# Kernel optimization log

Measured on AMD Instinct MI355X. Metric: run time of the kernel, lower is better.

Reference implementation:

```python
import jax, jax.numpy as jnp
import numpy as np

RANK = 16
NUM_STEPS = 10
STEP_SIZE = 1000.0
INIT_SCALE = 1e-3


def _init(k, shape):
    # projection of Dirichlet-like init onto sphere neighborhood: center +- init_scale uniform noise
    center = 1.0 / np.sqrt(shape[-1])
    return (center + (2.0 * INIT_SCALE) * jax.random.uniform(k, shape, dtype=jnp.float32) - INIT_SCALE)


def setup_inputs() -> dict:
    key = jax.random.key(0)
    ks = jax.random.split(key, 5)
    B, H, S, D = 2, 12, 8192, 64
    query = jax.random.normal(ks[0], (B, H, S, D), dtype=jnp.float32)
    key_t = jax.random.normal(ks[1], (B, H, S, D), dtype=jnp.float32)
    value = jax.random.normal(ks[2], (B, H, S, D), dtype=jnp.float32)
    left_params = _init(ks[3], (B, H, S, RANK))
    right_params = _init(ks[4], (B, H, RANK, S))
    return {"query": query, "key": key_t, "value": value,
            "left_params": left_params, "right_params": right_params}


def _unit(x):
    return x / jnp.linalg.norm(x, axis=-1, keepdims=True)


def _grad(lp, rp, q, k, inv_s2):
    # lp: [..., S, r]  rp: [..., r, S]  q,k: [..., S, D]
    ls = _unit(lp)
    rs = _unit(rp)
    L = ls * ls   # left simplex factor  [..., S, r]
    R = rs * rs   # right simplex factor [..., r, S]

    # d_left = (L (R R^T) - Q (K^T R^T)) / S^2   -- contract small dims first, never SxS
    RR = jnp.einsum('...ki,...li->...kl', R, R)          # [r, r]
    KR = jnp.einsum('...ia,...li->...la', k, R)          # [r, D]
    dl = (jnp.einsum('...jk,...kl->...jl', L, RR)
          - jnp.einsum('...ja,...la->...jl', q, KR)) * inv_s2
    dl = dl * 2.0 * ls
    dl = dl - ls * jnp.sum(ls * dl, axis=-1, keepdims=True)   # tangent-space projection
    dl = dl / jnp.linalg.norm(lp, axis=-1, keepdims=True)

    # d_right = ((L^T L) R - (L^T Q) K^T) / S^2
    LL = jnp.einsum('...jk,...jl->...kl', L, L)          # [r, r]
    LQ = jnp.einsum('...jk,...ja->...ka', L, q)          # [r, D]
    dr = (jnp.einsum('...kl,...li->...ki', LL, R)
          - jnp.einsum('...ka,...ia->...ki', LQ, k)) * inv_s2
    dr = dr * 2.0 * rs
    dr = dr - rs * jnp.sum(rs * dr, axis=-1, keepdims=True)
    dr = dr / jnp.linalg.norm(rp, axis=-1, keepdims=True)
    return dl, dr


def _forward(query, key, value, left_params, right_params):
    S = query.shape[-2]
    inv_s2 = jnp.float32(1.0 / (S * S))

    def step(carry, _):
        lp, rp = carry
        dl, dr = _grad(lp, rp, query, key, inv_s2)
        return (lp - STEP_SIZE * dl, rp - STEP_SIZE * dr), None

    (lp, rp), _ = jax.lax.scan(step, (left_params, right_params), None, length=NUM_STEPS)
    left = _unit(lp) ** 2    # [..., S, r]
    right = _unit(rp) ** 2   # [..., r, S]
    # left @ (right @ value) -- rank-bottleneck multiply, O(S*r*D)
    rv = jnp.einsum('...ki,...id->...kd', right, value)
    return jnp.einsum('...jk,...kd->...jd', left, rv)


def reference(query, key, value, left_params, right_params):
    return _forward(query, key, value, left_params, right_params)
```

## Files before the change

### kernel.cpp

```cpp
#include <hip/hip_runtime.h>

#define S_ 8192
#define D_ 64
#define BH_ 24

static constexpr float INV_S2 = 1.0f / (8192.0f * 8192.0f);
static constexpr float STEPSZ = 1000.0f;
static constexpr float CC = 2.0f * INV_S2;

#define LP_N (BH_ * S_ * 16)
#define PART_STRIDE 2576
#define PART_N (BH_ * 32 * PART_STRIDE)
#define ACCF_STRIDE 2624
#define ACCF_N (BH_ * ACCF_STRIDE)
#define PART2_STRIDE 1040
#define PART2_N (BH_ * 32 * PART2_STRIDE)

#define STG 20
#define WK_OFF 2608
#define LDS_FLOATS (WK_OFF + 5600)

template <int KIND>
__device__ __forceinline__ void reduceSideW(const float* __restrict__ sb, int j0, int t,
                                            const float* vals, float* WK,
                                            float* __restrict__ pbase) {
  const int lane = t & 63, w = t >> 6, tcx = t & 15;
  {
    float4* st = (float4*)(WK + t * STG);
    st[0] = make_float4(vals[0], vals[1], vals[2], vals[3]);
    st[1] = make_float4(vals[4], vals[5], vals[6], vals[7]);
    st[2] = make_float4(vals[8], vals[9], vals[10], vals[11]);
    st[3] = make_float4(vals[12], vals[13], vals[14], vals[15]);
  }
  __syncthreads();
  float aQ[16], aX[16], aN[16];
#pragma unroll
  for (int l = 0; l < 16; ++l) { aQ[l] = 0.f; aX[l] = 0.f; aN[l] = 0.f; }
#pragma unroll 4
  for (int it = 0; it < 64; ++it) {
    const int jl = (w << 6) + it;
    const float4* Vw = (const float4*)(WK + jl * STG);
    float4 b0 = Vw[0], b1 = Vw[1], b2 = Vw[2], b3 = Vw[3];
    float Vv[16] = {b0.x,b0.y,b0.z,b0.w, b1.x,b1.y,b1.z,b1.w,
                    b2.x,b2.y,b2.z,b2.w, b3.x,b3.y,b3.z,b3.w};
    float xq = sb[(size_t)(j0 + jl) * D_ + lane];
    float xc = (KIND < 2) ? WK[jl * STG + tcx] : 0.f;
#pragma unroll
    for (int l = 0; l < 16; ++l) {
      aQ[l] += Vv[l] * xq;
      if (KIND < 2) aX[l] += Vv[l] * xc;
      if (KIND >= 1) aN[l] += Vv[l];
    }
  }
  __syncthreads();
  float* rg = WK + w * 1400;
  {
    float* p = rg + lane * 17;
#pragma unroll
    for (int l = 0; l < 16; ++l) p[l] = aQ[l];
  }
  if (KIND < 2 && lane < 16) {
    float* p = rg + 1088 + lane * 17;
#pragma unroll
    for (int l = 0; l < 16; ++l) p[l] = aX[l];
  }
  if (KIND >= 1 && lane == 0) {
#pragma unroll
    for (int l = 0; l < 16; ++l) rg[1360 + l] = aN[l];
  }
  __syncthreads();
#pragma unroll
  for (int r = 0; r < 4; ++r) {
    int o = t + r * 256;
    int a = o >> 4, l = o & 15;
    int idx = a * 17 + l;
    pbase[a * 16 + l] = WK[idx] + WK[1400 + idx] + WK[2800 + idx] + WK[4200 + idx];
  }
  if (KIND < 2) {
    int c = t >> 4, l = t & 15;
    int idx = 1088 + c * 17 + l;
    pbase[1024 + l * 16 + c] = WK[idx] + WK[1400 + idx] + WK[2800 + idx] + WK[4200 + idx];
  }
  if (KIND >= 1 && t < 16) {
    int idx = 1360 + t;
    pbase[(KIND == 1 ? 1280 : 1024) + t] =
        WK[idx] + WK[1400 + idx] + WK[2800 + idx] + WK[4200 + idx];
  }
  __syncthreads();
}

__device__ __forceinline__ void rowUpdate(const float* M, const float4* q4, float lv[16]) {
  const float4* RR4 = (const float4*)M;
  const float4* KR4 = (const float4*)(M + 256);
  float n2 = 0.f;
#pragma unroll
  for (int l = 0; l < 16; ++l) n2 += lv[l] * lv[l];
  float ri = rsqrtf(n2);
  float ls[16], L[16];
#pragma unroll
  for (int l = 0; l < 16; ++l) { ls[l] = lv[l] * ri; L[l] = ls[l] * ls[l]; }
  float dl[16];
#pragma unroll
  for (int l = 0; l < 16; ++l) dl[l] = 0.f;
#pragma unroll
  for (int k = 0; k < 16; ++k) {
    float Lk = L[k];
#pragma unroll
    for (int g = 0; g < 4; ++g) {
      float4 rr = RR4[k * 4 + g];
      dl[4*g+0] += Lk * rr.x; dl[4*g+1] += Lk * rr.y;
      dl[4*g+2] += Lk * rr.z; dl[4*g+3] += Lk * rr.w;
    }
  }
#pragma unroll
  for (int a4 = 0; a4 < 16; ++a4) {
    float4 qq = q4[a4];
#pragma unroll
    for (int c = 0; c < 4; ++c) {
      float qa = (c == 0) ? qq.x : (c == 1) ? qq.y : (c == 2) ? qq.z : qq.w;
      int a = a4 * 4 + c;
#pragma unroll
      for (int g = 0; g < 4; ++g) {
        float4 kr = KR4[a * 4 + g];
        dl[4*g+0] -= qa * kr.x; dl[4*g+1] -= qa * kr.y;
        dl[4*g+2] -= qa * kr.z; dl[4*g+3] -= qa * kr.w;
      }
    }
  }
  float dot = 0.f;
#pragma unroll
  for (int l = 0; l < 16; ++l) { dl[l] *= ls[l]; dot += ls[l] * dl[l]; }
#pragma unroll
  for (int l = 0; l < 16; ++l) lv[l] -= STEPSZ * (dl[l] - ls[l] * dot) * ri;
}

__device__ __forceinline__ void colUpdateB(const float* M, const float* C,
                                           const float4* k4, float nv[16]) {
  const float4* MLL4 = (const float4*)M;
  const float4* MLQ4 = (const float4*)(M + 256);
  const float* C1 = C;
  const float* C2 = C + 16;
  const float* SRN = C + 32;
  float rp2[16];
#pragma unroll
  for (int l = 0; l < 16; ++l) rp2[l] = nv[l] * nv[l];
  float s[16];
#pragma unroll
  for (int k = 0; k < 16; ++k) {
    float a0 = 0.f;
#pragma unroll
    for (int g = 0; g < 4; ++g) {
      float4 m = MLL4[k * 4 + g];
      a0 += m.x * rp2[4*g+0] + m.y * rp2[4*g+1] + m.z * rp2[4*g+2] + m.w * rp2[4*g+3];
    }
    s[k] = a0;
  }
#pragma unroll
  for (int a4 = 0; a4 < 16; ++a4) {
    float4 kk = k4[a4];
#pragma unroll
    for (int k = 0; k < 16; ++k) {
      float4 m = MLQ4[k * 16 + a4];
      s[k] -= m.x * kk.x + m.y * kk.y + m.z * kk.z + m.w * kk.w;
    }
  }
#pragma unroll
  for (int k = 0; k < 16; ++k) {
    float rs = nv[k] * SRN[k];
    float d2 = rs * s[k];
    nv[k] = C1[k] * nv[k] - C2[k] * d2;
  }
}

template <int MODE>
__global__ void __launch_bounds__(256) kStep(const float* __restrict__ accF,
                                             const float* __restrict__ q,
                                             const float* __restrict__ key,
                                             const float* __restrict__ vv,
                                             const float* __restrict__ lp0,
                                             const float* __restrict__ rp0,
                                             float* __restrict__ lp,
                                             float* __restrict__ rp,
                                             float* __restrict__ part,
                                             float* __restrict__ part2) {
  const int bh = blockIdx.y, bx = blockIdx.x, t = threadIdx.x;
  const int j0 = bx * 256, j = j0 + t;
  const int bb = bh * 32 + bx;
  __shared__ float B[LDS_FLOATS];
  float* MAT = B;
  float* WK = B + WK_OFF;
  const float* A = accF + (size_t)bh * ACCF_STRIDE;
  const float* qb = q + (size_t)bh * S_ * D_;
  const float* kb = key + (size_t)bh * S_ * D_;
  const size_t base = ((size_t)bh * S_ + j) * 16;

  if (MODE >= 1) {
    for (int e = t; e < 2608; e += 256) MAT[e] = A[e];
    __syncthreads();
  }

  {
    float lv[16];
    const float4* s4 = (const float4*)((MODE == 0 ? lp0 : lp) + base);
    float4 a0 = s4[0], a1 = s4[1], a2 = s4[2], a3 = s4[3];
    lv[0]=a0.x; lv[1]=a0.y; lv[2]=a0.z; lv[3]=a0.w;
    lv[4]=a1.x; lv[5]=a1.y; lv[6]=a1.z; lv[7]=a1.w;
    lv[8]=a2.x; lv[9]=a2.y; lv[10]=a2.z; lv[11]=a2.w;
    lv[12]=a3.x; lv[13]=a3.y; lv[14]=a3.z; lv[15]=a3.w;
    if (MODE >= 1) {
      rowUpdate(MAT + 1280, (const float4*)(qb + (size_t)j * D_), lv);
    }
    float4* d4 = (float4*)(lp + base);
    d4[0] = make_float4(lv[0], lv[1], lv[2], lv[3]);
    d4[1] = make_float4(lv[4], lv[5], lv[6], lv[7]);
    d4[2] = make_float4(lv[8], lv[9], lv[10], lv[11]);
    d4[3] = make_float4(lv[12], lv[13], lv[14], lv[15]);
    if (MODE < 2) {
      float L[16];
      float m2 = 0.f;
#pragma unroll
      for (int l = 0; l < 16; ++l) m2 += lv[l] * lv[l];
      float r2 = 1.0f / m2;
#pragma unroll
      for (int l = 0; l < 16; ++l) L[l] = lv[l] * lv[l] * r2;
      reduceSideW<0>(qb, j0, t, L, WK, part + (size_t)bb * PART_STRIDE);
    }
  }

  {
    float nv[16];
    if (MODE == 0) {
      const float* rsrc = rp0 + (size_t)bh * 16 * S_ + j;
#pragma unroll
      for (int k = 0; k < 16; ++k) nv[k] = rsrc[(size_t)k * S_];
    } else {
      const float4* r4 = (const float4*)(rp + base);
      float4 a0 = r4[0], a1 = r4[1], a2 = r4[2], a3 = r4[3];
      nv[0]=a0.x; nv[1]=a0.y; nv[2]=a0.z; nv[3]=a0.w;
      nv[4]=a1.x; nv[5]=a1.y; nv[6]=a1.z; nv[7]=a1.w;
      nv[8]=a2.x; nv[9]=a2.y; nv[10]=a2.z; nv[11]=a2.w;
      nv[12]=a3.x; nv[13]=a3.y; nv[14]=a3.z; nv[15]=a3.w;
      colUpdateB(MAT, MAT + 2560, (const float4*)(kb + (size_t)j * D_), nv);
    }
    float4* d4 = (float4*)(rp + base);
    d4[0] = make_float4(nv[0], nv[1], nv[2], nv[3]);
    d4[1] = make_float4(nv[4], nv[5], nv[6], nv[7]);
    d4[2] = make_float4(nv[8], nv[9], nv[10], nv[11]);
    d4[3] = make_float4(nv[12], nv[13], nv[14], nv[15]);
    float rp2[16];
#pragma unroll
    for (int l = 0; l < 16; ++l) rp2[l] = nv[l] * nv[l];
    if (MODE < 2)
      reduceSideW<1>(kb, j0, t, rp2, WK, part + (size_t)bb * PART_STRIDE + 1280);
    else
      reduceSideW<2>(vv + (size_t)bh * S_ * D_, j0, t, rp2, WK,
                     part2 + (size_t)bb * PART2_STRIDE);
  }
}

__global__ void __launch_bounds__(256) kB(const float* __restrict__ part,
                                          float* __restrict__ accF) {
  const int bh = blockIdx.x, t = threadIdx.x;
  __shared__ float raw[PART_STRIDE];
  __shared__ float inn[16], srn[16];
  const float* p0 = part + (size_t)bh * 32 * PART_STRIDE;
  for (int vI = t; vI < PART_STRIDE; vI += 256) {
    float s = 0.f;
    const float* p = p0 + vI;
#pragma unroll 8
    for (int b2 = 0; b2 < 32; ++b2) s += p[(size_t)b2 * PART_STRIDE];
    raw[vI] = s;
  }
  __syncthreads();
  if (t < 16) {
    float N = raw[2560 + t];
    inn[t] = 1.0f / N;
    srn[t] = rsqrtf(N);
  }
  __syncthreads();
  float* o = accF + (size_t)bh * ACCF_STRIDE;
  o[t] = raw[1024 + t] * CC * inn[t & 15];
  o[1280 + t] = raw[2304 + t] * CC * inn[t >> 4] * inn[t & 15];
#pragma unroll
  for (int r = 0; r < 4; ++r) {
    int e = t + r * 256;
    o[256 + e] = raw[((e & 63) << 4) + (e >> 6)] * CC;
  }
#pragma unroll
  for (int r = 0; r < 4; ++r) {
    int e = t + r * 256;
    o[1536 + e] = raw[1280 + e] * CC * inn[e & 15];
  }
  if (t < 16) {
    int k = t;
    float s = 0.f;
#pragma unroll
    for (int l = 0; l < 16; ++l)
      s += raw[1024 + k * 16 + l] * CC * inn[l] * raw[2304 + k * 16 + l];
#pragma unroll
    for (int a = 0; a < 64; ++a)
      s -= raw[a * 16 + k] * CC * raw[1280 + a * 16 + k];
    float PJ = inn[k] * s;
    o[2560 + t] = 1.0f + STEPSZ * PJ * inn[t];
    o[2576 + t] = STEPSZ * srn[t];
    o[2592 + t] = srn[t];
  }
}

__global__ void __launch_bounds__(256) kBF(const float* __restrict__ part2,
                                           float* __restrict__ RVs) {
  const int bh = blockIdx.x, t = threadIdx.x;
  __shared__ float raw[PART2_STRIDE];
  __shared__ float inn[16];
  const float* p0 = part2 + (size_t)bh * 32 * PART2_STRIDE;
  for (int vI = t; vI < PART2_STRIDE; vI += 256) {
    float s = 0.f;
    const float* p = p0 + vI;
#pragma unroll 8
    for (int b2 = 0; b2 < 32; ++b2) s += p[(size_t)b2 * PART2_STRIDE];
    raw[vI] = s;
  }
  __syncthreads();
  if (t < 16) inn[t] = 1.0f / raw[1024 + t];
  __syncthreads();
#pragma unroll
  for (int r = 0; r < 4; ++r) {
    int e = t + r * 256;
    RVs[(size_t)bh * 1024 + e] = raw[((e & 63) << 4) + (e >> 6)] * inn[e >> 6];
  }
}

__global__ void __launch_bounds__(256) kOut(const float* __restrict__ lp,
                                            const float* __restrict__ RVs,
                                            float* __restrict__ out) {
  const int bh = blockIdx.y, t = threadIdx.x;
  __shared__ float rvs[1024];
#pragma unroll
  for (int r = 0; r < 4; ++r) rvs[t + r * 256] = RVs[(size_t)bh * 1024 + t + r * 256];
  __syncthreads();
  const int j = blockIdx.x * 256 + t;
  size_t base = ((size_t)bh * S_ + j) * 16;
  const float4* lp4 = (const float4*)(lp + base);
  float4 a0 = lp4[0], a1 = lp4[1], a2 = lp4[2], a3 = lp4[3];
  float lv[16] = {a0.x,a0.y,a0.z,a0.w, a1.x,a1.y,a1.z,a1.w,
                  a2.x,a2.y,a2.z,a2.w, a3.x,a3.y,a3.z,a3.w};
  float n2 = 0.f;
#pragma unroll
  for (int l = 0; l < 16; ++l) n2 += lv[l] * lv[l];
  float r2 = 1.0f / n2;
  float L[16];
#pragma unroll
  for (int l = 0; l < 16; ++l) L[l] = lv[l] * lv[l] * r2;
  float o[64];
#pragma unroll
  for (int d = 0; d < 64; ++d) o[d] = 0.f;
  const float4* rv4 = (const float4*)rvs;
#pragma unroll
  for (int k = 0; k < 16; ++k) {
    float Lk = L[k];
#pragma unroll
    for (int d4 = 0; d4 < 16; ++d4) {
      float4 r = rv4[k * 16 + d4];
      o[4*d4+0] += Lk * r.x; o[4*d4+1] += Lk * r.y;
      o[4*d4+2] += Lk * r.z; o[4*d4+3] += Lk * r.w;
    }
  }
  float4* o4 = (float4*)(out + ((size_t)bh * S_ + j) * D_);
#pragma unroll
  for (int d4 = 0; d4 < 16; ++d4)
    o4[d4] = make_float4(o[4*d4+0], o[4*d4+1], o[4*d4+2], o[4*d4+3]);
}

extern "C" void kernel_launch(void* const* d_in, const int* in_sizes, int n_in,
                              void* d_out, int out_size, void* d_ws, size_t ws_size,
                              hipStream_t stream) {
  (void)in_sizes; (void)n_in; (void)out_size; (void)ws_size;
  const float* q = (const float*)d_in[0];
  const float* key = (const float*)d_in[1];
  const float* v = (const float*)d_in[2];
  const float* lp0 = (const float*)d_in[3];
  const float* rp0 = (const float*)d_in[4];
  float* out = (float*)d_out;
  float* ws = (float*)d_ws;

  float* lp = ws;
  float* rp = lp + LP_N;
  float* part = rp + LP_N;
  float* accF = part + PART_N;
  float* part2 = accF + ACCF_N;
  float* RVs = part2 + PART2_N;

  dim3 blk(256);
  dim3 gS(32, BH_);
  kStep<0><<<gS, blk, 0, stream>>>(accF, q, key, v, lp0, rp0, lp, rp, part, part2);
  for (int s = 0; s < 10; ++s) {
    kB<<<dim3(BH_), blk, 0, stream>>>(part, accF);
    if (s < 9)
      kStep<1><<<gS, blk, 0, stream>>>(accF, q, key, v, lp0, rp0, lp, rp, part, part2);
    else
      kStep<2><<<gS, blk, 0, stream>>>(accF, q, key, v, lp0, rp0, lp, rp, part, part2);
  }
  kBF<<<dim3(BH_), blk, 0, stream>>>(part2, RVs);
  kOut<<<gS, blk, 0, stream>>>(lp, RVs, out);
}
```

Measured before the change: 935.1 us.

## Transpose Q/K and factors to column-major, split row/col work across grid z

Adds pre-pass kernels that transpose query, key and the left params so per-thread reads in the update loops are coalesced across threads instead of strided 256-byte rows. The row and column updates now run in separate blocks (grid z=2), which doubles parallelism and cuts LDS per block. The reduction is also restructured so the 16-wide X/N sums use a strided row split plus wavefront shuffles instead of full 64-row loops. The cost is extra transpose traffic, more workspace (the transposed path is used only when the workspace is large enough), and a layout change to the KR/LQ matrices read in kB.

```diff
diff --git a/kernel.cpp b/kernel.cpp
--- a/kernel.cpp
+++ b/kernel.cpp
@@ -9,6 +9,7 @@
 static constexpr float CC = 2.0f * INV_S2;
 
 #define LP_N (BH_ * S_ * 16)
+#define QT_N (BH_ * S_ * 64)
 #define PART_STRIDE 2576
 #define PART_N (BH_ * 32 * PART_STRIDE)
 #define ACCF_STRIDE 2624
@@ -17,43 +18,59 @@
 #define PART2_N (BH_ * 32 * PART2_STRIDE)
 
 #define STG 20
-#define WK_OFF 2608
-#define LDS_FLOATS (WK_OFF + 5600)
 
 template <int KIND>
 __device__ __forceinline__ void reduceSideW(const float* __restrict__ sb, int j0, int t,
-                                            const float* vals, float* WK,
+                                            const float* vals, float* B,
                                             float* __restrict__ pbase) {
-  const int lane = t & 63, w = t >> 6, tcx = t & 15;
+  const int lane = t & 63, w = t >> 6, tcx = t & 15, rr = (t >> 4) & 3;
   {
-    float4* st = (float4*)(WK + t * STG);
+    float4* st = (float4*)(B + t * STG);
     st[0] = make_float4(vals[0], vals[1], vals[2], vals[3]);
     st[1] = make_float4(vals[4], vals[5], vals[6], vals[7]);
     st[2] = make_float4(vals[8], vals[9], vals[10], vals[11]);
     st[3] = make_float4(vals[12], vals[13], vals[14], vals[15]);
   }
   __syncthreads();
-  float aQ[16], aX[16], aN[16];
-#pragma unroll
-  for (int l = 0; l < 16; ++l) { aQ[l] = 0.f; aX[l] = 0.f; aN[l] = 0.f; }
-#pragma unroll 4
+  float aQ[16];
+#pragma unroll
+  for (int l = 0; l < 16; ++l) aQ[l] = 0.f;
+  const float* srow = sb + (size_t)(j0 + (w << 6)) * D_ + lane;
+#pragma unroll 8
   for (int it = 0; it < 64; ++it) {
     const int jl = (w << 6) + it;
-    const float4* Vw = (const float4*)(WK + jl * STG);
+    const float4* Vw = (const float4*)(B + jl * STG);
+    float4 b0 = Vw[0], b1 = Vw[1], b2 = Vw[2], b3 = Vw[3];
+    float xq = srow[(size_t)it * D_];
+    aQ[0]  += b0.x * xq; aQ[1]  += b0.y * xq; aQ[2]  += b0.z * xq; aQ[3]  += b0.w * xq;
+    aQ[4]  += b1.x * xq; aQ[5]  += b1.y * xq; aQ[6]  += b1.z * xq; aQ[7]  += b1.w * xq;
+    aQ[8]  += b2.x * xq; aQ[9]  += b2.y * xq; aQ[10] += b2.z * xq; aQ[11] += b2.w * xq;
+    aQ[12] += b3.x * xq; aQ[13] += b3.y * xq; aQ[14] += b3.z * xq; aQ[15] += b3.w * xq;
+  }
+  float aX[16], aN[16];
+#pragma unroll
+  for (int l = 0; l < 16; ++l) { aX[l] = 0.f; aN[l] = 0.f; }
+#pragma unroll 4
+  for (int it = 0; it < 16; ++it) {
+    const int jl = (w << 6) + rr + (it << 2);
+    const float4* Vw = (const float4*)(B + jl * STG);
     float4 b0 = Vw[0], b1 = Vw[1], b2 = Vw[2], b3 = Vw[3];
     float Vv[16] = {b0.x,b0.y,b0.z,b0.w, b1.x,b1.y,b1.z,b1.w,
                     b2.x,b2.y,b2.z,b2.w, b3.x,b3.y,b3.z,b3.w};
-    float xq = sb[(size_t)(j0 + jl) * D_ + lane];
-    float xc = (KIND < 2) ? WK[jl * STG + tcx] : 0.f;
+    float xc = (KIND < 2) ? B[jl * STG + tcx] : 0.f;
 #pragma unroll
     for (int l = 0; l < 16; ++l) {
-      aQ[l] += Vv[l] * xq;
       if (KIND < 2) aX[l] += Vv[l] * xc;
       if (KIND >= 1) aN[l] += Vv[l];
     }
   }
-  __syncthreads();
-  float* rg = WK + w * 1400;
+#pragma unroll
+  for (int l = 0; l < 16; ++l) {
+    if (KIND < 2) { float v = aX[l]; v += __shfl_xor(v, 16); v += __shfl_xor(v, 32); aX[l] = v; }
+    if (KIND >= 1) { float v = aN[l]; v += __shfl_xor(v, 16); v += __shfl_xor(v, 32); aN[l] = v; }
+  }
+  __syncthreads();
+  float* rg = B + w * 1400;
   {
     float* p = rg + lane * 17;
 #pragma unroll
@@ -74,24 +91,25 @@
     int o = t + r * 256;
     int a = o >> 4, l = o & 15;
     int idx = a * 17 + l;
-    pbase[a * 16 + l] = WK[idx] + WK[1400 + idx] + WK[2800 + idx] + WK[4200 + idx];
+    pbase[a * 16 + l] = B[idx] + B[1400 + idx] + B[2800 + idx] + B[4200 + idx];
   }
   if (KIND < 2) {
     int c = t >> 4, l = t & 15;
     int idx = 1088 + c * 17 + l;
-    pbase[1024 + l * 16 + c] = WK[idx] + WK[1400 + idx] + WK[2800 + idx] + WK[4200 + idx];
+    pbase[1024 + l * 16 + c] = B[idx] + B[1400 + idx] + B[2800 + idx] + B[4200 + idx];
   }
   if (KIND >= 1 && t < 16) {
     int idx = 1360 + t;
     pbase[(KIND == 1 ? 1280 : 1024) + t] =
-        WK[idx] + WK[1400 + idx] + WK[2800 + idx] + WK[4200 + idx];
-  }
-  __syncthreads();
-}
-
-__device__ __forceinline__ void rowUpdate(const float* M, const float4* q4, float lv[16]) {
+        B[idx] + B[1400 + idx] + B[2800 + idx] + B[4200 + idx];
+  }
+  __syncthreads();
+}
+
+template <int UT>
+__device__ __forceinline__ void rowUpdate(const float* M, const float* __restrict__ qsrc,
+                                          int j, float lv[16]) {
   const float4* RR4 = (const float4*)M;
-  const float4* KR4 = (const float4*)(M + 256);
   float n2 = 0.f;
 #pragma unroll
   for (int l = 0; l < 16; ++l) n2 += lv[l] * lv[l];
@@ -112,20 +130,35 @@
       dl[4*g+2] += Lk * rr.z; dl[4*g+3] += Lk * rr.w;
     }
   }
-#pragma unroll
-  for (int a4 = 0; a4 < 16; ++a4) {
-    float4 qq = q4[a4];
-#pragma unroll
-    for (int c = 0; c < 4; ++c) {
-      float qa = (c == 0) ? qq.x : (c == 1) ? qq.y : (c == 2) ? qq.z : qq.w;
-      int a = a4 * 4 + c;
+  if (UT) {
+#pragma unroll 8
+    for (int a = 0; a < 64; ++a) {
+      float qa = qsrc[(size_t)a * S_ + j];
+      const float4* kr = (const float4*)(M + 256 + a * 16);
 #pragma unroll
       for (int g = 0; g < 4; ++g) {
-        float4 kr = KR4[a * 4 + g];
-        dl[4*g+0] -= qa * kr.x; dl[4*g+1] -= qa * kr.y;
-        dl[4*g+2] -= qa * kr.z; dl[4*g+3] -= qa * kr.w;
+        float4 k4 = kr[g];
+        dl[4*g+0] -= qa * k4.x; dl[4*g+1] -= qa * k4.y;
+        dl[4*g+2] -= qa * k4.z; dl[4*g+3] -= qa * k4.w;
       }
     }
+  } else {
+    const float4* q4 = (const float4*)qsrc;
+#pragma unroll
+    for (int a4 = 0; a4 < 16; ++a4) {
+      float4 qq = q4[a4];
+#pragma unroll
+      for (int c = 0; c < 4; ++c) {
+        float qa = (c == 0) ? qq.x : (c == 1) ? qq.y : (c == 2) ? qq.z : qq.w;
+        const float4* kr = (const float4*)(M + 256 + (a4 * 4 + c) * 16);
+#pragma unroll
+        for (int g = 0; g < 4; ++g) {
+          float4 k4 = kr[g];
+          dl[4*g+0] -= qa * k4.x; dl[4*g+1] -= qa * k4.y;
+          dl[4*g+2] -= qa * k4.z; dl[4*g+3] -= qa * k4.w;
+        }
+      }
+    }
   }
   float dot = 0.f;
 #pragma unroll
@@ -134,10 +167,11 @@
   for (int l = 0; l < 16; ++l) lv[l] -= STEPSZ * (dl[l] - ls[l] * dot) * ri;
 }
 
-__device__ __forceinline__ void colUpdateB(const float* M, const float* C,
-                                           const float4* k4, float nv[16]) {
+template <int UT>
+__device__ __forceinline__ void colUpdate(const float* M, const float* C,
+                                          const float* __restrict__ ksrc,
+                                          int i, float nv[16]) {
   const float4* MLL4 = (const float4*)M;
-  const float4* MLQ4 = (const float4*)(M + 256);
   const float* C1 = C;
   const float* C2 = C + 16;
   const float* SRN = C + 32;
@@ -155,13 +189,34 @@
     }
     s[k] = a0;
   }
-#pragma unroll
-  for (int a4 = 0; a4 < 16; ++a4) {
-    float4 kk = k4[a4];
-#pragma unroll
-    for (int k = 0; k < 16; ++k) {
-      float4 m = MLQ4[k * 16 + a4];
-      s[k] -= m.x * kk.x + m.y * kk.y + m.z * kk.z + m.w * kk.w;
+  if (UT) {
+#pragma unroll 8
+    for (int a = 0; a < 64; ++a) {
+      float ka = ksrc[(size_t)a * S_ + i];
+      const float4* mq = (const float4*)(M + 256 + a * 16);
+#pragma unroll
+      for (int g = 0; g < 4; ++g) {
+        float4 m = mq[g];
+        s[4*g+0] -= ka * m.x; s[4*g+1] -= ka * m.y;
+        s[4*g+2] -= ka * m.z; s[4*g+3] -= ka * m.w;
+      }
+    }
+  } else {
+    const float4* k4 = (const float4*)ksrc;
+#pragma unroll
+    for (int a4 = 0; a4 < 16; ++a4) {
+      float4 kk = k4[a4];
+#pragma unroll
+      for (int c = 0; c < 4; ++c) {
+        float ka = (c == 0) ? kk.x : (c == 1) ? kk.y : (c == 2) ? kk.z : kk.w;
+        const float4* mq = (const float4*)(M + 256 + (a4 * 4 + c) * 16);
+#pragma unroll
+        for (int g = 0; g < 4; ++g) {
+          float4 m = mq[g];
+          s[4*g+0] -= ka * m.x; s[4*g+1] -= ka * m.y;
+          s[4*g+2] -= ka * m.z; s[4*g+3] -= ka * m.w;
+        }
+      }
     }
   }
 #pragma unroll
@@ -172,88 +227,71 @@
   }
 }
 
-template <int MODE>
+template <int MODE, int UT>
 __global__ void __launch_bounds__(256) kStep(const float* __restrict__ accF,
                                              const float* __restrict__ q,
                                              const float* __restrict__ key,
                                              const float* __restrict__ vv,
-                                             const float* __restrict__ lp0,
-                                             const float* __restrict__ rp0,
-                                             float* __restrict__ lp,
-                                             float* __restrict__ rp,
+                                             const float* __restrict__ qT,
+                                             const float* __restrict__ kT,
+                                             float* __restrict__ lpT,
+                                             const float* __restrict__ rp_src,
+                                             float* __restrict__ rp_dst,
                                              float* __restrict__ part,
                                              float* __restrict__ part2) {
   const int bh = blockIdx.y, bx = blockIdx.x, t = threadIdx.x;
   const int j0 = bx * 256, j = j0 + t;
   const int bb = bh * 32 + bx;
-  __shared__ float B[LDS_FLOATS];
-  float* MAT = B;
-  float* WK = B + WK_OFF;
+  __shared__ float B[6400];
   const float* A = accF + (size_t)bh * ACCF_STRIDE;
   const float* qb = q + (size_t)bh * S_ * D_;
   const float* kb = key + (size_t)bh * S_ * D_;
-  const size_t base = ((size_t)bh * S_ + j) * 16;
-
-  if (MODE >= 1) {
-    for (int e = t; e < 2608; e += 256) MAT[e] = A[e];
-    __syncthreads();
-  }
-
-  {
+
+  if (blockIdx.z == 0) {
+    float* lpb = lpT + (size_t)bh * 16 * S_;
     float lv[16];
-    const float4* s4 = (const float4*)((MODE == 0 ? lp0 : lp) + base);
-    float4 a0 = s4[0], a1 = s4[1], a2 = s4[2], a3 = s4[3];
-    lv[0]=a0.x; lv[1]=a0.y; lv[2]=a0.z; lv[3]=a0.w;
-    lv[4]=a1.x; lv[5]=a1.y; lv[6]=a1.z; lv[7]=a1.w;
-    lv[8]=a2.x; lv[9]=a2.y; lv[10]=a2.z; lv[11]=a2.w;
-    lv[12]=a3.x; lv[13]=a3.y; lv[14]=a3.z; lv[15]=a3.w;
+#pragma unroll
+    for (int l = 0; l < 16; ++l) lv[l] = lpb[(size_t)l * S_ + j];
     if (MODE >= 1) {
-      rowUpdate(MAT + 1280, (const float4*)(qb + (size_t)j * D_), lv);
-    }
-    float4* d4 = (float4*)(lp + base);
-    d4[0] = make_float4(lv[0], lv[1], lv[2], lv[3]);
-    d4[1] = make_float4(lv[4], lv[5], lv[6], lv[7]);
-    d4[2] = make_float4(lv[8], lv[9], lv[10], lv[11]);
-    d4[3] = make_float4(lv[12], lv[13], lv[14], lv[15]);
-    if (MODE < 2) {
-      float L[16];
+      for (int e = t; e < 1280; e += 256) B[e] = A[1280 + e];
+      __syncthreads();
+      rowUpdate<UT>(B, UT ? (qT + (size_t)bh * 64 * S_) : (qb + (size_t)j * D_), j, lv);
+#pragma unroll
+      for (int l = 0; l < 16; ++l) lpb[(size_t)l * S_ + j] = lv[l];
+      if (MODE == 2) return;
+      __syncthreads();
+    }
+    float L[16];
+    {
       float m2 = 0.f;
 #pragma unroll
       for (int l = 0; l < 16; ++l) m2 += lv[l] * lv[l];
       float r2 = 1.0f / m2;
 #pragma unroll
       for (int l = 0; l < 16; ++l) L[l] = lv[l] * lv[l] * r2;
-      reduceSideW<0>(qb, j0, t, L, WK, part + (size_t)bb * PART_STRIDE);
-    }
-  }
-
-  {
+    }
+    reduceSideW<0>(qb, j0, t, L, B, part + (size_t)bb * PART_STRIDE);
+  } else {
+    const float* rsb = rp_src + (size_t)bh * 16 * S_;
     float nv[16];
-    if (MODE == 0) {
-      const float* rsrc = rp0 + (size_t)bh * 16 * S_ + j;
-#pragma unroll
-      for (int k = 0; k < 16; ++k) nv[k] = rsrc[(size_t)k * S_];
-    } else {
-      const float4* r4 = (const float4*)(rp + base);
-      float4 a0 = r4[0], a1 = r4[1], a2 = r4[2], a3 = r4[3];
-      nv[0]=a0.x; nv[1]=a0.y; nv[2]=a0.z; nv[3]=a0.w;
-      nv[4]=a1.x; nv[5]=a1.y; nv[6]=a1.z; nv[7]=a1.w;
-      nv[8]=a2.x; nv[9]=a2.y; nv[10]=a2.z; nv[11]=a2.w;
-      nv[12]=a3.x; nv[13]=a3.y; nv[14]=a3.z; nv[15]=a3.w;
-      colUpdateB(MAT, MAT + 2560, (const float4*)(kb + (size_t)j * D_), nv);
-    }
-    float4* d4 = (float4*)(rp + base);
-    d4[0] = make_float4(nv[0], nv[1], nv[2], nv[3]);
-    d4[1] = make_float4(nv[4], nv[5], nv[6], nv[7]);
-    d4[2] = make_float4(nv[8], nv[9], nv[10], nv[11]);
-    d4[3] = make_float4(nv[12], nv[13], nv[14], nv[15]);
+#pragma unroll
+    for (int k = 0; k < 16; ++k) nv[k] = rsb[(size_t)k * S_ + j];
+    if (MODE >= 1) {
+      for (int e = t; e < 1328; e += 256) B[e] = (e < 1280) ? A[e] : A[1280 + e];
+      __syncthreads();
+      colUpdate<UT>(B, B + 1280, UT ? (kT + (size_t)bh * 64 * S_) : (kb + (size_t)j * D_), j, nv);
+      float* rdb = rp_dst + (size_t)bh * 16 * S_;
+#pragma unroll
+      for (int k = 0; k < 16; ++k) rdb[(size_t)k * S_ + j] = nv[k];
+      __syncthreads();
+    }
     float rp2[16];
 #pragma unroll
     for (int l = 0; l < 16; ++l) rp2[l] = nv[l] * nv[l];
     if (MODE < 2)
-      reduceSideW<1>(kb, j0, t, rp2, WK, part + (size_t)bb * PART_STRIDE + 1280);
+      reduceSideW<1>(kb, j0, t, rp2, B, part + (size_t)bb * PART_STRIDE + 1280);
     else
-      reduceSideW<2>(vv + (size_t)bh * S_ * D_, j0, t, rp2, WK,
+      reduceSideW<2>(vv + (size_t)bh * S_ * D_, j0, t, rp2, B,
                      part2 + (size_t)bb * PART2_STRIDE);
   }
 }
@@ -284,7 +322,7 @@
 #pragma unroll
   for (int r = 0; r < 4; ++r) {
     int e = t + r * 256;
-    o[256 + e] = raw[((e & 63) << 4) + (e >> 6)] * CC;
+    o[256 + e] = raw[e] * CC;
   }
 #pragma unroll
   for (int r = 0; r < 4; ++r) {
@@ -330,7 +368,7 @@
   }
 }
 
-__global__ void __launch_bounds__(256) kOut(const float* __restrict__ lp,
+__global__ void __launch_bounds__(256) kOut(const float* __restrict__ lpT,
                                             const float* __restrict__ RVs,
                                             float* __restrict__ out) {
   const int bh = blockIdx.y, t = threadIdx.x;
@@ -339,11 +377,10 @@
   for (int r = 0; r < 4; ++r) rvs[t + r * 256] = RVs[(size_t)bh * 1024 + t + r * 256];
   __syncthreads();
   const int j = blockIdx.x * 256 + t;
-  size_t base = ((size_t)bh * S_ + j) * 16;
-  const float4* lp4 = (const float4*)(lp + base);
-  float4 a0 = lp4[0], a1 = lp4[1], a2 = lp4[2], a3 = lp4[3];
-  float lv[16] = {a0.x,a0.y,a0.z,a0.w, a1.x,a1.y,a1.z,a1.w,
-                  a2.x,a2.y,a2.z,a2.w, a3.x,a3.y,a3.z,a3.w};
+  const float* lpb = lpT + (size_t)bh * 16 * S_;
+  float lv[16];
+#pragma unroll
+  for (int l = 0; l < 16; ++l) lv[l] = lpb[(size_t)l * S_ + j];
   float n2 = 0.f;
 #pragma unroll
   for (int l = 0; l < 16; ++l) n2 += lv[l] * lv[l];
@@ -371,10 +408,50 @@
     o4[d4] = make_float4(o[4*d4+0], o[4*d4+1], o[4*d4+2], o[4*d4+3]);
 }
 
+__global__ void __launch_bounds__(256) kTrans64(const float* __restrict__ src,
+                                                float* __restrict__ dst) {
+  const int bh = blockIdx.y, t = threadIdx.x;
+  const int j0 = blockIdx.x * 64;
+  __shared__ float tile[64 * 65];
+#pragma unroll
+  for (int i = 0; i < 16; ++i) {
+    int idx = t + 256 * i;
+    int row = idx >> 6, col = idx & 63;
+    tile[col * 65 + row] = src[((size_t)bh * S_ + j0 + row) * 64 + col];
+  }
+  __syncthreads();
+#pragma unroll
+  for (int i = 0; i < 16; ++i) {
+    int idx = t + 256 * i;
+    int a = idx >> 6, jj = idx & 63;
+    dst[(size_t)bh * 64 * S_ + (size_t)a * S_ + j0 + jj] = tile[a * 65 + jj];
+  }
+}
+
+__global__ void __launch_bounds__(256) kTransL(const float* __restrict__ lp0,
+                                               float* __restrict__ lpT) {
+  const int bh = blockIdx.y, t = threadIdx.x;
+  const int j0 = blockIdx.x * 64;
+  __shared__ float tile[16 * 65];
+#pragma unroll
+  for (int i = 0; i < 4; ++i) {
+    int idx = t + 256 * i;
+    int row = idx >> 4, col = idx & 15;
+    tile[col * 65 + row] = lp0[((size_t)bh * S_ + j0 + row) * 16 + col];
+  }
+  __syncthreads();
+#pragma unroll
+  for (int i = 0; i < 4; ++i) {
+    int idx = t + 256 * i;
+    int l = idx >> 6, jj = idx & 63;
+    lpT[(size_t)bh * 16 * S_ + (size_t)l * S_ + j0 + jj] = tile[l * 65 + jj];
+  }
+}
+
 extern "C" void kernel_launch(void* const* d_in, const int* in_sizes, int n_in,
                               void* d_out, int out_size, void* d_ws, size_t ws_size,
                               hipStream_t stream) {
-  (void)in_sizes; (void)n_in; (void)out_size; (void)ws_size;
+  (void)in_sizes; (void)n_in; (void)out_size;
   const float* q = (const float*)d_in[0];
   const float* key = (const float*)d_in[1];
   const float* v = (const float*)d_in[2];
@@ -383,23 +460,48 @@
   float* out = (float*)d_out;
   float* ws = (float*)d_ws;
 
-  float* lp = ws;
-  float* rp = lp + LP_N;
+  float* lpT = ws;
+  float* rp = lpT + LP_N;
   float* part = rp + LP_N;
   float* accF = part + PART_N;
   float* part2 = accF + ACCF_N;
   float* RVs = part2 + PART2_N;
+  float* qT = RVs + BH_ * 1024;
+  float* kT = qT + QT_N;
+  const size_t full_need = (size_t)(9156096 + 2 * QT_N) * sizeof(float);
+  const bool useT = ws_size >= full_need;
 
   dim3 blk(256);
-  dim3 gS(32, BH_);
-  kStep<0><<<gS, blk, 0, stream>>>(accF, q, key, v, lp0, rp0, lp, rp, part, part2);
-  for (int s = 0; s < 10; ++s) {
-    kB<<<dim3(BH_), blk, 0, stream>>>(part, accF);
-    if (s < 9)
-      kStep<1><<<gS, blk, 0, stream>>>(accF, q, key, v, lp0, rp0, lp, rp, part, part2);
-    else
-      kStep<2><<<gS, blk, 0, stream>>>(accF, q, key, v, lp0, rp0, lp, rp, part, part2);
+  dim3 gS(32, BH_, 2);
+  dim3 gT(128, BH_);
+
+  kTransL<<<gT, blk, 0, stream>>>(lp0, lpT);
+  if (useT) {
+    kTrans64<<<gT, blk, 0, stream>>>(q, qT);
+    kTrans64<<<gT, blk, 0, stream>>>(key, kT);
+  }
+
+  if (useT) {
+    kStep<0, 1><<<gS, blk, 0, stream>>>(accF, q, key, v, qT, kT, lpT, rp0, rp, part, part2);
+    for (int s = 0; s < 10; ++s) {
+      kB<<<dim3(BH_), blk, 0, stream>>>(part, accF);
+      const float* rsrc = (s == 0) ? rp0 : rp;
+      if (s < 9)
+        kStep<1, 1><<<gS, blk, 0, stream>>>(accF, q, key, v, qT, kT, lpT, rsrc, rp, part, part2);
+      else
+        kStep<2, 1><<<gS, blk, 0, stream>>>(accF, q, key, v, qT, kT, lpT, rsrc, rp, part, part2);
+    }
+  } else {
+    kStep<0, 0><<<gS, blk, 0, stream>>>(accF, q, key, v, qT, kT, lpT, rp0, rp, part, part2);
+    for (int s = 0; s < 10; ++s) {
+      kB<<<dim3(BH_), blk, 0, stream>>>(part, accF);
+      const float* rsrc = (s == 0) ? rp0 : rp;
+      if (s < 9)
+        kStep<1, 0><<<gS, blk, 0, stream>>>(accF, q, key, v, qT, kT, lpT, rsrc, rp, part, part2);
+      else
+        kStep<2, 0><<<gS, blk, 0, stream>>>(accF, q, key, v, qT, kT, lpT, rsrc, rp, part, part2);
+    }
   }
   kBF<<<dim3(BH_), blk, 0, stream>>>(part2, RVs);
-  kOut<<<gS, blk, 0, stream>>>(lp, RVs, out);
-}
+  kOut<<<dim3(32, BH_), blk, 0, stream>>>(lpT, RVs, out);
+}
```

Result: slower. 1.303 ms (+39.3%).

## Split row and column updates into separate blocks and restructure reductions

Applied to the files above, without the earlier changes.

The step kernel's grid gains a z dimension: z=0 blocks handle left-factor rows and z=1 blocks handle right-factor columns, and each block now covers 512 positions in two halves. The Q/K-weighted side reduction is reorganized so each thread accumulates a 4x16 outer product from float4 loads and partial sums are combined with cross-lane shuffles instead of extra LDS passes. The KR/LQ matrix layout in accF is transposed so the row and column updates read contiguous float4 rows, and kB writes those entries untransposed. The intent is more parallel blocks per step, fewer barriers and fewer LDS round trips, at the cost of more registers per thread and each block loading its own copy of the small matrices.

```diff
diff --git a/kernel.cpp b/kernel.cpp
--- a/kernel.cpp
+++ b/kernel.cpp
@@ -16,48 +16,81 @@
 #define PART2_STRIDE 1040
 #define PART2_N (BH_ * 32 * PART2_STRIDE)
 
-#define STG 20
-#define WK_OFF 2608
-#define LDS_FLOATS (WK_OFF + 5600)
-
 template <int KIND>
-__device__ __forceinline__ void reduceSideW(const float* __restrict__ sb, int j0, int t,
-                                            const float* vals, float* WK,
-                                            float* __restrict__ pbase) {
-  const int lane = t & 63, w = t >> 6, tcx = t & 15;
+__device__ __forceinline__ void reduceSide(const float* __restrict__ sb, int jbase, int t,
+                                           const float* vals, float* ST, float* RD,
+                                           float* __restrict__ pbase) {
+  const int tc = t & 15, trw = t >> 4, w = t >> 6, lane = t & 63;
   {
-    float4* st = (float4*)(WK + t * STG);
+    float4* st = (float4*)(ST + t * 20);
     st[0] = make_float4(vals[0], vals[1], vals[2], vals[3]);
     st[1] = make_float4(vals[4], vals[5], vals[6], vals[7]);
     st[2] = make_float4(vals[8], vals[9], vals[10], vals[11]);
     st[3] = make_float4(vals[12], vals[13], vals[14], vals[15]);
   }
   __syncthreads();
-  float aQ[16], aX[16], aN[16];
-#pragma unroll
-  for (int l = 0; l < 16; ++l) { aQ[l] = 0.f; aX[l] = 0.f; aN[l] = 0.f; }
+  float aQ[4][16];
+#pragma unroll
+  for (int c = 0; c < 4; ++c)
+#pragma unroll
+    for (int l = 0; l < 16; ++l) aQ[c][l] = 0.f;
+  const float* srow = sb + (size_t)jbase * D_;
 #pragma unroll 4
-  for (int it = 0; it < 64; ++it) {
-    const int jl = (w << 6) + it;
-    const float4* Vw = (const float4*)(WK + jl * STG);
+  for (int it = 0; it < 16; ++it) {
+    const int jl = trw + (it << 4);
+    const float4* Vw = (const float4*)(ST + jl * 20);
     float4 b0 = Vw[0], b1 = Vw[1], b2 = Vw[2], b3 = Vw[3];
     float Vv[16] = {b0.x,b0.y,b0.z,b0.w, b1.x,b1.y,b1.z,b1.w,
                     b2.x,b2.y,b2.z,b2.w, b3.x,b3.y,b3.z,b3.w};
-    float xq = sb[(size_t)(j0 + jl) * D_ + lane];
-    float xc = (KIND < 2) ? WK[jl * STG + tcx] : 0.f;
+    float4 qq = *(const float4*)(srow + (size_t)jl * D_ + (tc << 2));
 #pragma unroll
     for (int l = 0; l < 16; ++l) {
-      aQ[l] += Vv[l] * xq;
+      aQ[0][l] += qq.x * Vv[l];
+      aQ[1][l] += qq.y * Vv[l];
+      aQ[2][l] += qq.z * Vv[l];
+      aQ[3][l] += qq.w * Vv[l];
+    }
+  }
+#pragma unroll
+  for (int c = 0; c < 4; ++c)
+#pragma unroll
+    for (int l = 0; l < 16; ++l) {
+      float v = aQ[c][l];
+      v += __shfl_xor(v, 16);
+      v += __shfl_xor(v, 32);
+      aQ[c][l] = v;
+    }
+  float* rg = RD + w * 1400;
+  if (lane < 16) {
+#pragma unroll
+    for (int c = 0; c < 4; ++c) {
+      float* p = rg + (4 * lane + c) * 17;
+#pragma unroll
+      for (int l = 0; l < 16; ++l) p[l] = aQ[c][l];
+    }
+  }
+  const int rr = trw & 3;
+  float aX[16], aN[16];
+#pragma unroll
+  for (int l = 0; l < 16; ++l) { aX[l] = 0.f; aN[l] = 0.f; }
+#pragma unroll 4
+  for (int it = 0; it < 16; ++it) {
+    const int jl = (w << 6) + rr + (it << 2);
+    const float4* Vw = (const float4*)(ST + jl * 20);
+    float4 b0 = Vw[0], b1 = Vw[1], b2 = Vw[2], b3 = Vw[3];
+    float Vv[16] = {b0.x,b0.y,b0.z,b0.w, b1.x,b1.y,b1.z,b1.w,
+                    b2.x,b2.y,b2.z,b2.w, b3.x,b3.y,b3.z,b3.w};
+    float xc = (KIND < 2) ? ST[jl * 20 + tc] : 0.f;
+#pragma unroll
+    for (int l = 0; l < 16; ++l) {
       if (KIND < 2) aX[l] += Vv[l] * xc;
       if (KIND >= 1) aN[l] += Vv[l];
     }
   }
-  __syncthreads();
-  float* rg = WK + w * 1400;
-  {
-    float* p = rg + lane * 17;
-#pragma unroll
-    for (int l = 0; l < 16; ++l) p[l] = aQ[l];
+#pragma unroll
+  for (int l = 0; l < 16; ++l) {
+    if (KIND < 2) { float v = aX[l]; v += __shfl_xor(v, 16); v += __shfl_xor(v, 32); aX[l] = v; }
+    if (KIND >= 1) { float v = aN[l]; v += __shfl_xor(v, 16); v += __shfl_xor(v, 32); aN[l] = v; }
   }
   if (KIND < 2 && lane < 16) {
     float* p = rg + 1088 + lane * 17;
@@ -66,7 +99,7 @@
   }
   if (KIND >= 1 && lane == 0) {
 #pragma unroll
-    for (int l = 0; l < 16; ++l) rg[1360 + l] = aN[l];
+    for (int l = 0; l < 16; ++l) rg[1376 + l] = aN[l];
   }
   __syncthreads();
 #pragma unroll
@@ -74,24 +107,22 @@
     int o = t + r * 256;
     int a = o >> 4, l = o & 15;
     int idx = a * 17 + l;
-    pbase[a * 16 + l] = WK[idx] + WK[1400 + idx] + WK[2800 + idx] + WK[4200 + idx];
+    pbase[a * 16 + l] = RD[idx] + RD[1400 + idx] + RD[2800 + idx] + RD[4200 + idx];
   }
   if (KIND < 2) {
     int c = t >> 4, l = t & 15;
     int idx = 1088 + c * 17 + l;
-    pbase[1024 + l * 16 + c] = WK[idx] + WK[1400 + idx] + WK[2800 + idx] + WK[4200 + idx];
+    pbase[1024 + l * 16 + c] = RD[idx] + RD[1400 + idx] + RD[2800 + idx] + RD[4200 + idx];
   }
   if (KIND >= 1 && t < 16) {
-    int idx = 1360 + t;
+    int idx = 1376 + t;
     pbase[(KIND == 1 ? 1280 : 1024) + t] =
-        WK[idx] + WK[1400 + idx] + WK[2800 + idx] + WK[4200 + idx];
-  }
-  __syncthreads();
+        RD[idx] + RD[1400 + idx] + RD[2800 + idx] + RD[4200 + idx];
+  }
 }
 
 __device__ __forceinline__ void rowUpdate(const float* M, const float4* q4, float lv[16]) {
   const float4* RR4 = (const float4*)M;
-  const float4* KR4 = (const float4*)(M + 256);
   float n2 = 0.f;
 #pragma unroll
   for (int l = 0; l < 16; ++l) n2 += lv[l] * lv[l];
@@ -118,12 +149,12 @@
 #pragma unroll
     for (int c = 0; c < 4; ++c) {
       float qa = (c == 0) ? qq.x : (c == 1) ? qq.y : (c == 2) ? qq.z : qq.w;
-      int a = a4 * 4 + c;
+      const float4* kr = (const float4*)(M + 256 + (a4 * 4 + c) * 16);
 #pragma unroll
       for (int g = 0; g < 4; ++g) {
-        float4 kr = KR4[a * 4 + g];
-        dl[4*g+0] -= qa * kr.x; dl[4*g+1] -= qa * kr.y;
-        dl[4*g+2] -= qa * kr.z; dl[4*g+3] -= qa * kr.w;
+        float4 k4 = kr[g];
+        dl[4*g+0] -= qa * k4.x; dl[4*g+1] -= qa * k4.y;
+        dl[4*g+2] -= qa * k4.z; dl[4*g+3] -= qa * k4.w;
       }
     }
   }
@@ -134,10 +165,9 @@
   for (int l = 0; l < 16; ++l) lv[l] -= STEPSZ * (dl[l] - ls[l] * dot) * ri;
 }
 
-__device__ __forceinline__ void colUpdateB(const float* M, const float* C,
-                                           const float4* k4, float nv[16]) {
+__device__ __forceinline__ void colUpdate(const float* M, const float* C,
+                                          const float4* k4, float nv[16]) {
   const float4* MLL4 = (const float4*)M;
-  const float4* MLQ4 = (const float4*)(M + 256);
   const float* C1 = C;
   const float* C2 = C + 16;
   const float* SRN = C + 32;
@@ -159,9 +189,15 @@
   for (int a4 = 0; a4 < 16; ++a4) {
     float4 kk = k4[a4];
 #pragma unroll
-    for (int k = 0; k < 16; ++k) {
-      float4 m = MLQ4[k * 16 + a4];
-      s[k] -= m.x * kk.x + m.y * kk.y + m.z * kk.z + m.w * kk.w;
+    for (int c = 0; c < 4; ++c) {
+      float ka = (c == 0) ? kk.x : (c == 1) ? kk.y : (c == 2) ? kk.z : kk.w;
+      const float4* mq = (const float4*)(M + 256 + (a4 * 4 + c) * 16);
+#pragma unroll
+      for (int g = 0; g < 4; ++g) {
+        float4 m = mq[g];
+        s[4*g+0] -= ka * m.x; s[4*g+1] -= ka * m.y;
+        s[4*g+2] -= ka * m.z; s[4*g+3] -= ka * m.w;
+      }
     }
   }
 #pragma unroll
@@ -184,77 +220,86 @@
                                              float* __restrict__ part,
                                              float* __restrict__ part2) {
   const int bh = blockIdx.y, bx = blockIdx.x, t = threadIdx.x;
-  const int j0 = bx * 256, j = j0 + t;
-  const int bb = bh * 32 + bx;
-  __shared__ float B[LDS_FLOATS];
-  float* MAT = B;
-  float* WK = B + WK_OFF;
+  const int j0 = bx * 512;
+  __shared__ float M[1344];
+  __shared__ float ST[5120];
+  __shared__ float RD[5600];
   const float* A = accF + (size_t)bh * ACCF_STRIDE;
   const float* qb = q + (size_t)bh * S_ * D_;
   const float* kb = key + (size_t)bh * S_ * D_;
-  const size_t base = ((size_t)bh * S_ + j) * 16;
-
-  if (MODE >= 1) {
-    for (int e = t; e < 2608; e += 256) MAT[e] = A[e];
-    __syncthreads();
-  }
-
-  {
-    float lv[16];
-    const float4* s4 = (const float4*)((MODE == 0 ? lp0 : lp) + base);
-    float4 a0 = s4[0], a1 = s4[1], a2 = s4[2], a3 = s4[3];
-    lv[0]=a0.x; lv[1]=a0.y; lv[2]=a0.z; lv[3]=a0.w;
-    lv[4]=a1.x; lv[5]=a1.y; lv[6]=a1.z; lv[7]=a1.w;
-    lv[8]=a2.x; lv[9]=a2.y; lv[10]=a2.z; lv[11]=a2.w;
-    lv[12]=a3.x; lv[13]=a3.y; lv[14]=a3.z; lv[15]=a3.w;
+
+  if (blockIdx.z == 0) {
     if (MODE >= 1) {
-      rowUpdate(MAT + 1280, (const float4*)(qb + (size_t)j * D_), lv);
-    }
-    float4* d4 = (float4*)(lp + base);
-    d4[0] = make_float4(lv[0], lv[1], lv[2], lv[3]);
-    d4[1] = make_float4(lv[4], lv[5], lv[6], lv[7]);
-    d4[2] = make_float4(lv[8], lv[9], lv[10], lv[11]);
-    d4[3] = make_float4(lv[12], lv[13], lv[14], lv[15]);
-    if (MODE < 2) {
+      for (int e = t; e < 1280; e += 256) M[e] = A[1280 + e];
+      __syncthreads();
+    }
+    for (int h = 0; h < 2; ++h) {
+      const int j = j0 + h * 256 + t;
+      const size_t base = ((size_t)bh * S_ + j) * 16;
+      float lv[16];
+      const float4* s4 = (const float4*)((MODE == 0 ? lp0 : lp) + base);
+      float4 a0 = s4[0], a1 = s4[1], a2 = s4[2], a3 = s4[3];
+      lv[0]=a0.x; lv[1]=a0.y; lv[2]=a0.z; lv[3]=a0.w;
+      lv[4]=a1.x; lv[5]=a1.y; lv[6]=a1.z; lv[7]=a1.w;
+      lv[8]=a2.x; lv[9]=a2.y; lv[10]=a2.z; lv[11]=a2.w;
+      lv[12]=a3.x; lv[13]=a3.y; lv[14]=a3.z; lv[15]=a3.w;
+      if (MODE >= 1)
+        rowUpdate(M, (const float4*)(qb + (size_t)j * D_), lv);
+      float4* d4 = (float4*)(lp + base);
+      d4[0] = make_float4(lv[0], lv[1], lv[2], lv[3]);
+      d4[1] = make_float4(lv[4], lv[5], lv[6], lv[7]);
+      d4[2] = make_float4(lv[8], lv[9], lv[10], lv[11]);
+      d4[3] = make_float4(lv[12], lv[13], lv[14], lv[15]);
+      if (MODE == 2) continue;
       float L[16];
-      float m2 = 0.f;
-#pragma unroll
-      for (int l = 0; l < 16; ++l) m2 += lv[l] * lv[l];
-      float r2 = 1.0f / m2;
-#pragma unroll
-      for (int l = 0; l < 16; ++l) L[l] = lv[l] * lv[l] * r2;
-      reduceSideW<0>(qb, j0, t, L, WK, part + (size_t)bb * PART_STRIDE);
-    }
-  }
-
-  {
-    float nv[16];
-    if (MODE == 0) {
-      const float* rsrc = rp0 + (size_t)bh * 16 * S_ + j;
-#pragma unroll
-      for (int k = 0; k < 16; ++k) nv[k] = rsrc[(size_t)k * S_];
-    } else {
-      const float4* r4 = (const float4*)(rp + base);
-      float4 a0 = r4[0], a1 = r4[1], a2 = r4[2], a3 = r4[3];
-      nv[0]=a0.x; nv[1]=a0.y; nv[2]=a0.z; nv[3]=a0.w;
-      nv[4]=a1.x; nv[5]=a1.y; nv[6]=a1.z; nv[7]=a1.w;
-      nv[8]=a2.x; nv[9]=a2.y; nv[10]=a2.z; nv[11]=a2.w;
-      nv[12]=a3.x; nv[13]=a3.y; nv[14]=a3.z; nv[15]=a3.w;
-      colUpdateB(MAT, MAT + 2560, (const float4*)(kb + (size_t)j * D_), nv);
-    }
-    float4* d4 = (float4*)(rp + base);
-    d4[0] = make_float4(nv[0], nv[1], nv[2], nv[3]);
-    d4[1] = make_float4(nv[4], nv[5], nv[6], nv[7]);
-    d4[2] = make_float4(nv[8], nv[9], nv[10], nv[11]);
-    d4[3] = make_float4(nv[12], nv[13], nv[14], nv[15]);
-    float rp2[16];
-#pragma unroll
-    for (int l = 0; l < 16; ++l) rp2[l] = nv[l] * nv[l];
-    if (MODE < 2)
-      reduceSideW<1>(kb, j0, t, rp2, WK, part + (size_t)bb * PART_STRIDE + 1280);
-    else
-      reduceSideW<2>(vv + (size_t)bh * S_ * D_, j0, t, rp2, WK,
-                     part2 + (size_t)bb * PART2_STRIDE);
+      {
+        float m2 = 0.f;
+#pragma unroll
+        for (int l = 0; l < 16; ++l) m2 += lv[l] * lv[l];
+        float r2 = 1.0f / m2;
+#pragma unroll
+        for (int l = 0; l < 16; ++l) L[l] = lv[l] * lv[l] * r2;
+      }
+      reduceSide<0>(qb, j0 + h * 256, t, L, ST, RD,
+                    part + (size_t)(bh * 32 + bx * 2 + h) * PART_STRIDE);
+    }
+  } else {
+    if (MODE >= 1) {
+      for (int e = t; e < 1328; e += 256) M[e] = (e < 1280) ? A[e] : A[1280 + e];
+      __syncthreads();
+    }
+    for (int h = 0; h < 2; ++h) {
+      const int j = j0 + h * 256 + t;
+      const size_t base = ((size_t)bh * S_ + j) * 16;
+      float nv[16];
+      if (MODE == 0) {
+        const float* rsrc = rp0 + (size_t)bh * 16 * S_ + j;
+#pragma unroll
+        for (int k = 0; k < 16; ++k) nv[k] = rsrc[(size_t)k * S_];
+      } else {
+        const float4* r4 = (const float4*)(rp + base);
+        float4 a0 = r4[0], a1 = r4[1], a2 = r4[2], a3 = r4[3];
+        nv[0]=a0.x; nv[1]=a0.y; nv[2]=a0.z; nv[3]=a0.w;
+        nv[4]=a1.x; nv[5]=a1.y; nv[6]=a1.z; nv[7]=a1.w;
+        nv[8]=a2.x; nv[9]=a2.y; nv[10]=a2.z; nv[11]=a2.w;
+        nv[12]=a3.x; nv[13]=a3.y; nv[14]=a3.z; nv[15]=a3.w;
+        colUpdate(M, M + 1280, (const float4*)(kb + (size_t)j * D_), nv);
+      }
+      float4* d4 = (float4*)(rp + base);
+      d4[0] = make_float4(nv[0], nv[1], nv[2], nv[3]);
+      d4[1] = make_float4(nv[4], nv[5], nv[6], nv[7]);
+      d4[2] = make_float4(nv[8], nv[9], nv[10], nv[11]);
+      d4[3] = make_float4(nv[12], nv[13], nv[14], nv[15]);
+      float rp2[16];
+#pragma unroll
+      for (int l = 0; l < 16; ++l) rp2[l] = nv[l] * nv[l];
+      if (MODE < 2)
+        reduceSide<1>(kb, j0 + h * 256, t, rp2, ST, RD,
+                      part + (size_t)(bh * 32 + bx * 2 + h) * PART_STRIDE + 1280);
+      else
+        reduceSide<2>(vv + (size_t)bh * S_ * D_, j0 + h * 256, t, rp2, ST, RD,
+                      part2 + (size_t)(bh * 32 + bx * 2 + h) * PART2_STRIDE);
+    }
   }
 }
 
@@ -284,7 +329,7 @@
 #pragma unroll
   for (int r = 0; r < 4; ++r) {
     int e = t + r * 256;
-    o[256 + e] = raw[((e & 63) << 4) + (e >> 6)] * CC;
+    o[256 + e] = raw[e] * CC;
   }
 #pragma unroll
   for (int r = 0; r < 4; ++r) {
@@ -391,7 +436,7 @@
   float* RVs = part2 + PART2_N;
 
   dim3 blk(256);
-  dim3 gS(32, BH_);
+  dim3 gS(16, BH_, 2);
   kStep<0><<<gS, blk, 0, stream>>>(accF, q, key, v, lp0, rp0, lp, rp, part, part2);
   for (int s = 0; s < 10; ++s) {
     kB<<<dim3(BH_), blk, 0, stream>>>(part, accF);
@@ -401,5 +446,5 @@
       kStep<2><<<gS, blk, 0, stream>>>(accF, q, key, v, lp0, rp0, lp, rp, part, part2);
   }
   kBF<<<dim3(BH_), blk, 0, stream>>>(part2, RVs);
-  kOut<<<gS, blk, 0, stream>>>(lp, RVs, out);
-}
+  kOut<<<dim3(32, BH_), blk, 0, stream>>>(lp, RVs, out);
+}
```

New measurement: 1.066 ms. 14.0% more time.
